# Kernel tuning notes

Measured on AMD Instinct MI355X. Metric: run time of the kernel, lower is better.

The kernel has to match this reference:

```python
import jax, jax.numpy as jnp
import numpy as np

WIN = 16
HEADS = 4


def _window_partition(x, win):
    B, H, W, C = x.shape
    x = x.reshape(B, H // win, win, W // win, win, C)
    x = x.transpose(0, 1, 3, 2, 4, 5)
    return x.reshape(-1, win * win, C)


def _reverse_window_partition(x, win, H, W):
    N, _, C = x.shape
    x = x.reshape(-1, H // win, W // win, win, win, C)
    x = x.transpose(0, 1, 3, 2, 4, 5)
    return x.reshape(-1, H, W, C)


def setup_inputs() -> dict:
    key = jax.random.key(0)
    ks = jax.random.split(key, 7)
    B, H, W, C = 2, 256, 256, 96
    s = 0.02
    return {
        "x": jax.random.normal(ks[0], (B, H, W, C), jnp.float32),
        "qkv_w": jax.random.normal(ks[1], (C, 3 * C), jnp.float32) * s,
        "qkv_b": jax.random.normal(ks[2], (3 * C,), jnp.float32) * s,
        "pe_w": jax.random.normal(ks[3], (3, 3, 1, C), jnp.float32) * s,  # depthwise HWIO
        "pe_b": jax.random.normal(ks[4], (C,), jnp.float32) * s,
        "out_w": jax.random.normal(ks[5], (C, C), jnp.float32) * s,
        "out_b": jax.random.normal(ks[6], (C,), jnp.float32) * s,
    }


def reference(x, qkv_w, qkv_b, pe_w, pe_b, out_w, out_b):
    B, H, W, C = x.shape
    win, heads = WIN, HEADS
    hd = C // heads

    z = _window_partition(x, win)
    N, S, _ = z.shape

    qkv = z @ qkv_w + qkv_b                       # (N, S, 3C)
    # headify then chunk(3): each head's 3*hd channels split into q,k,v
    qkv = qkv.reshape(N, S, heads, 3, hd).transpose(0, 2, 3, 1, 4)  # (N, h, 3, S, hd)
    q, k, v = qkv[:, :, 0], qkv[:, :, 1], qkv[:, :, 2]

    # Locally-enhanced PE: depthwise 3x3 conv on de-headified v
    v_img = v.transpose(0, 2, 1, 3).reshape(N, win, win, C)  # NHWC
    lepe = jax.lax.conv_general_dilated(
        v_img, pe_w, (1, 1), 'SAME',
        dimension_numbers=('NHWC', 'HWIO', 'NHWC'),
        feature_group_count=C) + pe_b
    lepe = lepe.reshape(N, S, heads, hd).transpose(0, 2, 1, 3)  # (N, h, S, hd)

    # per-window SDPA (default scale 1/sqrt(hd))
    scale = 1.0 / jnp.sqrt(jnp.asarray(hd, x.dtype))
    attn = jax.nn.softmax(jnp.einsum('nhsd,nhtd->nhst', q, k) * scale, axis=-1)
    o = jnp.einsum('nhst,nhtd->nhsd', attn, v) + lepe

    o = o.transpose(0, 2, 1, 3).reshape(N, S, C)
    o = _reverse_window_partition(o, win, H, W)   # (B, H, W, C)
    return o @ out_w + out_b
```

## Files before the change

### kernel.cpp

```cpp
#include <hip/hip_runtime.h>


typedef __attribute__((ext_vector_type(8))) short bf16x8;
typedef __attribute__((ext_vector_type(4))) float f32x4;

#define MFMA(a, b, c) __builtin_amdgcn_mfma_f32_16x16x32_bf16(a, b, c, 0, 0, 0)

#if __has_builtin(__builtin_amdgcn_exp2f)
#define EXP2F(x) __builtin_amdgcn_exp2f(x)
#else
#define EXP2F(x) exp2f(x)
#endif

#define SCALE2 (0.20412414523193154f * 1.4426950408889634f)

#define OFF_WT   0u
#define OFF_B2   55296u
#define OFF_WTO  56448u
#define OFF_Q    75904u
#define OFF_K    25241728u
#define OFF_VT   50407552u

__device__ __forceinline__ unsigned short f2bf(float f) {
    union { float f; unsigned int u; } v; v.f = f;
    unsigned int u = v.u;
    return (unsigned short)((u + 0x7FFFu + ((u >> 16) & 1u)) >> 16);
}
__device__ __forceinline__ float bf2f(unsigned short h) {
    union { unsigned int u; float f; } v; v.u = ((unsigned int)h) << 16;
    return v.f;
}
__device__ __forceinline__ unsigned int pk2bf(float a, float b) {
#if __has_builtin(__builtin_amdgcn_cvt_pk_bf16_f32)
    auto p = __builtin_amdgcn_cvt_pk_bf16_f32(a, b);
    union { decltype(p) v; unsigned int u; } cv; cv.v = p;
    return cv.u;
#else
    return (unsigned int)f2bf(a) | ((unsigned int)f2bf(b) << 16);
#endif
}
__device__ __forceinline__ float frcp(float x) {
#if __has_builtin(__builtin_amdgcn_rcpf)
    return __builtin_amdgcn_rcpf(x);
#else
    return 1.0f / x;
#endif
}

__global__ void prep_kernel(const float* __restrict__ qkv_w,
                            const float* __restrict__ qkv_b,
                            const float* __restrict__ out_w,
                            unsigned short* __restrict__ wt,
                            float* __restrict__ b2,
                            unsigned short* __restrict__ wto) {
    const int stride = gridDim.x * 256;
    int i0 = blockIdx.x * 256 + threadIdx.x;
    for (int i = i0; i < 288 * 96; i += stride) {
        const int c = i / 96, k = i % 96;
        float v = qkv_w[k * 288 + c];
        if ((c % 72) < 24) v *= SCALE2;
        wt[i] = f2bf(v);
    }
    for (int i = i0; i < 288; i += stride) {
        float v = qkv_b[i];
        if ((i % 72) < 24) v *= SCALE2;
        b2[i] = v;
    }
    for (int i = i0; i < 96 * 96; i += stride) {
        const int c = i / 96, k = i % 96;
        wto[i] = f2bf(out_w[k * 96 + c]);
    }
}

__launch_bounds__(256, 4)
__global__ void qkv_kernel(const float* __restrict__ x,
                           const unsigned short* __restrict__ wt,
                           const float* __restrict__ b2,
                           unsigned short* __restrict__ Qb,
                           unsigned short* __restrict__ Kb,
                           unsigned short* __restrict__ VTb) {
    __shared__ unsigned short z[128 * 104];
    const int blk = blockIdx.x;
    const int n = blk >> 1, half = blk & 1;
    const int T0 = half << 7;
    const int tid = threadIdx.x;
    const int bW = n >> 8, hy = (n >> 4) & 15, wx = n & 15;

    for (int i = tid; i < 128 * 24; i += 256) {
        const int tl = i / 24, c4 = i % 24;
        const int tok = T0 + tl;
        const int y = tok >> 4, xx = tok & 15;
        const size_t row = (size_t)((bW * 256 + hy * 16 + y) * 256 + wx * 16 + xx);
        const float4 v = *(const float4*)(x + row * 96 + c4 * 4);
        uint2 pk; pk.x = pk2bf(v.x, v.y); pk.y = pk2bf(v.z, v.w);
        *(uint2*)&z[tl * 104 + c4 * 4] = pk;
    }
    __syncthreads();

    const int w = tid >> 6, l = tid & 63;
    const int lm = l & 15, lq = l >> 4;

    bf16x8 af[3][3];
#pragma unroll
    for (int mt = 0; mt < 3; mt++)
#pragma unroll
        for (int ks = 0; ks < 3; ks++)
            af[mt][ks] = *(const bf16x8*)(wt + (w * 72 + mt * 16 + lm) * 96 + ks * 32 + lq * 8);

    for (int nt = 0; nt < 8; nt++) {
        bf16x8 bz[3];
#pragma unroll
        for (int ks = 0; ks < 3; ks++)
            bz[ks] = *(const bf16x8*)&z[(nt * 16 + lm) * 104 + ks * 32 + lq * 8];
#pragma unroll
        for (int mt = 0; mt < 3; mt++) {
            f32x4 acc = {0.f, 0.f, 0.f, 0.f};
#pragma unroll
            for (int ks = 0; ks < 3; ks++) acc = MFMA(af[mt][ks], bz[ks], acc);
            const int r48 = mt * 16 + lq * 4;
            const float4 bias = *(const float4*)(b2 + w * 72 + r48);
            const int kind = r48 / 24, idx = r48 % 24;
            const int tok = T0 + nt * 16 + lm;
            uint2 pk;
            pk.x = pk2bf(acc[0] + bias.x, acc[1] + bias.y);
            pk.y = pk2bf(acc[2] + bias.z, acc[3] + bias.w);
            unsigned short* dst = kind ? Kb : Qb;
            *(uint2*)(dst + ((size_t)(n * 4 + w) * 256 + tok) * 24 + idx) = pk;
        }
    }

#pragma unroll
    for (int tt2 = 0; tt2 < 2; tt2++) {
        const int gtt = w * 2 + tt2;
        bf16x8 az[3];
#pragma unroll
        for (int ks = 0; ks < 3; ks++)
            az[ks] = *(const bf16x8*)&z[(gtt * 16 + lm) * 104 + ks * 32 + lq * 8];
#pragma unroll
        for (int nv = 0; nv < 6; nv++) {
            const int j = nv * 16 + lm;
            const int vrow = (j / 24) * 72 + 48 + (j % 24);
            f32x4 acc = {0.f, 0.f, 0.f, 0.f};
#pragma unroll
            for (int ks = 0; ks < 3; ks++) {
                const bf16x8 bw = *(const bf16x8*)(wt + vrow * 96 + ks * 32 + lq * 8);
                acc = MFMA(az[ks], bw, acc);
            }
            const float bv = b2[vrow];
            const int tokb = T0 + gtt * 16 + lq * 4;
            uint2 pk;
            pk.x = pk2bf(acc[0] + bv, acc[1] + bv);
            pk.y = pk2bf(acc[2] + bv, acc[3] + bv);
            *(uint2*)(VTb + ((size_t)(n * 4 + j / 24) * 24 + (j % 24)) * 256 + tokb) = pk;
        }
    }
}

__launch_bounds__(256, 2)
__global__ void attn_out_kernel(const unsigned short* __restrict__ Qb,
                                const unsigned short* __restrict__ Kb,
                                const unsigned short* __restrict__ VTb,
                                const float* __restrict__ pe_w,
                                const float* __restrict__ pe_b,
                                const unsigned short* __restrict__ wto,
                                const float* __restrict__ out_b,
                                float* __restrict__ out) {
    __shared__ unsigned short sVT[32 * 264];
    __shared__ unsigned short sPO[4 * 64 * 40];
    __shared__ float sPW[216];
    __shared__ float sPB[24];

    const int n = blockIdx.x, tid = threadIdx.x;
    const int w = tid >> 6, l = tid & 63;
    const int lm = l & 15, lq = l >> 4;
    const int qbase = w * 64;
    unsigned short* Pw = &sPO[w * 64 * 40];

    f32x4 oacc[4][6];
#pragma unroll
    for (int b = 0; b < 4; b++)
#pragma unroll
        for (int nt = 0; nt < 6; nt++) oacc[b][nt] = (f32x4){0.f, 0.f, 0.f, 0.f};

    for (int h = 0; h < 4; h++) {
        const size_t nh = (size_t)(n * 4 + h);
        __syncthreads();
        for (int i = tid; i < 24 * 64; i += 256) {
            const int row = i >> 6, c = i & 63;
            *(ushort4*)&sVT[row * 264 + c * 4] =
                *(const ushort4*)(VTb + (nh * 24 + row) * 256 + c * 4);
        }
        if (tid < 64) {
            ushort4 ones; ones.x = ones.y = ones.z = ones.w = (unsigned short)0x3F80;
            *(ushort4*)&sVT[24 * 264 + tid * 4] = ones;
        }
        for (int i = tid; i < 216; i += 256) sPW[i] = pe_w[(i / 24) * 96 + h * 24 + (i % 24)];
        if (tid < 24) sPB[tid] = pe_b[h * 24 + tid];

        bf16x8 qf[4];
#pragma unroll
        for (int b = 0; b < 4; b++) {
            bf16x8 qv = *(const bf16x8*)(Qb + (nh * 256 + qbase + b * 16 + lm) * 24 + lq * 8);
            if (lq == 3) qv = (bf16x8)(short)0;
            qf[b] = qv;
        }
        __syncthreads();

        f32x4 oa[4][2];
#pragma unroll
        for (int b = 0; b < 4; b++)
#pragma unroll
            for (int c = 0; c < 2; c++) oa[b][c] = (f32x4){0.f, 0.f, 0.f, 0.f};

        bf16x8 kfn[2];
#pragma unroll
        for (int a = 0; a < 2; a++)
            kfn[a] = *(const bf16x8*)(Kb + (nh * 256 + a * 16 + lm) * 24 + lq * 8);

        for (int kc = 0; kc < 8; kc++) {
            bf16x8 kfc[2] = {kfn[0], kfn[1]};
            if (kc < 7) {
#pragma unroll
                for (int a = 0; a < 2; a++)
                    kfn[a] = *(const bf16x8*)(Kb + (nh * 256 + (kc + 1) * 32 + a * 16 + lm) * 24 + lq * 8);
            }
#pragma unroll
            for (int a = 0; a < 2; a++) {
                f32x4 s[4];
#pragma unroll
                for (int b = 0; b < 4; b++)
                    s[b] = MFMA(kfc[a], qf[b], ((f32x4){0.f, 0.f, 0.f, 0.f}));
#pragma unroll
                for (int b = 0; b < 4; b++) {
                    uint2 pk;
                    pk.x = pk2bf(EXP2F(s[b][0]), EXP2F(s[b][1]));
                    pk.y = pk2bf(EXP2F(s[b][2]), EXP2F(s[b][3]));
                    *(uint2*)&Pw[(b * 16 + lm) * 40 + a * 16 + lq * 4] = pk;
                }
            }
            bf16x8 vb[2];
#pragma unroll
            for (int c = 0; c < 2; c++)
                vb[c] = *(const bf16x8*)&sVT[(c * 16 + lm) * 264 + kc * 32 + lq * 8];
#pragma unroll
            for (int b = 0; b < 4; b++) {
                const bf16x8 pa = *(const bf16x8*)&Pw[(b * 16 + lm) * 40 + lq * 8];
#pragma unroll
                for (int c = 0; c < 2; c++) oa[b][c] = MFMA(pa, vb[c], oa[b][c]);
            }
        }

        {
            uint4 zz = {0u, 0u, 0u, 0u};
            *(uint4*)&Pw[l * 40 + 24] = zz;
        }
        float w9[2][9], pb2[2];
#pragma unroll
        for (int c = 0; c < 2; c++) {
            const int ch = c * 16 + lm;
            if (ch < 24) {
#pragma unroll
                for (int ta = 0; ta < 9; ta++) w9[c][ta] = sPW[ta * 24 + ch];
                pb2[c] = sPB[ch];
            }
        }
#pragma unroll
        for (int b = 0; b < 4; b++) {
            float rinv[4];
#pragma unroll
            for (int r = 0; r < 4; r++)
                rinv[r] = frcp(__shfl(oa[b][1][r], (l & 48) | 8, 64));
            const int y = w * 4 + b;
            const int x0 = lq * 4;
#pragma unroll
            for (int c = 0; c < 2; c++) {
                const int ch = c * 16 + lm;
                if (ch < 24) {
                    float lep[4] = {pb2[c], pb2[c], pb2[c], pb2[c]};
                    const unsigned short* vbase = &sVT[ch * 264];
#pragma unroll
                    for (int dy = -1; dy <= 1; dy++) {
                        const int ny = y + dy;
                        if ((unsigned)ny > 15u) continue;
                        const unsigned short* vrow = vbase + ny * 16;
                        const float wl = w9[c][(dy + 1) * 3 + 0];
                        const float wm = w9[c][(dy + 1) * 3 + 1];
                        const float wr = w9[c][(dy + 1) * 3 + 2];
#pragma unroll
                        for (int d = -1; d <= 4; d++) {
                            const int xx = x0 + d;
                            if ((unsigned)xx > 15u) continue;
                            const float v = bf2f(vrow[xx]);
                            if (d - 1 >= 0 && d - 1 <= 3) lep[d - 1] = fmaf(v, wr, lep[d - 1]);
                            if (d >= 0 && d <= 3)         lep[d]     = fmaf(v, wm, lep[d]);
                            if (d + 1 <= 3)               lep[d + 1] = fmaf(v, wl, lep[d + 1]);
                        }
                    }
#pragma unroll
                    for (int r = 0; r < 4; r++) {
                        const float val = oa[b][c][r] * rinv[r] + lep[r];
                        Pw[(b * 16 + lq * 4 + r) * 40 + ch] = f2bf(val);
                    }
                }
            }
        }

        bf16x8 aO[4];
#pragma unroll
        for (int b = 0; b < 4; b++)
            aO[b] = *(const bf16x8*)&Pw[(b * 16 + lm) * 40 + lq * 8];
#pragma unroll
        for (int nt = 0; nt < 6; nt++) {
            const bf16x8 bwf = *(const bf16x8*)(wto + (nt * 16 + lm) * 96 + h * 24 + lq * 8);
#pragma unroll
            for (int b = 0; b < 4; b++) oacc[b][nt] = MFMA(aO[b], bwf, oacc[b][nt]);
        }
    }

    const int bW = n >> 8, hy = (n >> 4) & 15, wx = n & 15;
#pragma unroll
    for (int nt = 0; nt < 6; nt++) {
        const float bias = out_b[nt * 16 + lm];
#pragma unroll
        for (int b = 0; b < 4; b++) {
#pragma unroll
            for (int r = 0; r < 4; r++) {
                const int t = qbase + b * 16 + lq * 4 + r;
                const size_t grow =
                    (size_t)((bW * 256 + hy * 16 + (t >> 4)) * 256 + wx * 16 + (t & 15));
                out[grow * 96 + nt * 16 + lm] = oacc[b][nt][r] + bias;
            }
        }
    }
}

extern "C" void kernel_launch(void* const* d_in, const int* in_sizes, int n_in,
                              void* d_out, int out_size, void* d_ws, size_t ws_size,
                              hipStream_t stream) {
    const float* x     = (const float*)d_in[0];
    const float* qkv_w = (const float*)d_in[1];
    const float* qkv_b = (const float*)d_in[2];
    const float* pe_w  = (const float*)d_in[3];
    const float* pe_b  = (const float*)d_in[4];
    const float* out_w = (const float*)d_in[5];
    const float* out_b = (const float*)d_in[6];
    float* out = (float*)d_out;

    char* ws = (char*)d_ws;
    unsigned short* wt  = (unsigned short*)(ws + OFF_WT);
    float*          b2  = (float*)(ws + OFF_B2);
    unsigned short* wto = (unsigned short*)(ws + OFF_WTO);
    unsigned short* Qb  = (unsigned short*)(ws + OFF_Q);
    unsigned short* Kb  = (unsigned short*)(ws + OFF_K);
    unsigned short* VTb = (unsigned short*)(ws + OFF_VT);

    prep_kernel<<<72, 256, 0, stream>>>(qkv_w, qkv_b, out_w, wt, b2, wto);
    qkv_kernel<<<1024, 256, 0, stream>>>(x, wt, b2, Qb, Kb, VTb);
    attn_out_kernel<<<512, 256, 0, stream>>>(Qb, Kb, VTb, pe_w, pe_b, wto, out_b, out);
}
```

Baseline: 201.1 us.

## Fuse QKV projection into attention kernel, keeping Q/K/V in shared memory

Removes the separate qkv_kernel and its global-memory round trip for Q, K and V^T. Each attention block now loads its window of x into registers as bf16 fragments and computes per-head Q, K and V with MFMA. The results go straight into shared-memory buffers used by the attention loop. This avoids writing and re-reading roughly 75 MB of intermediates and one kernel launch. In exchange it adds shared-memory and register pressure, plus redundant weight loads per head inside the block, which may lower occupancy.

```diff
diff --git a/kernel.cpp b/kernel.cpp
--- a/kernel.cpp
+++ b/kernel.cpp
@@ -17,9 +17,6 @@
 #define OFF_WT   0u
 #define OFF_B2   55296u
 #define OFF_WTO  56448u
-#define OFF_Q    75904u
-#define OFF_K    25241728u
-#define OFF_VT   50407552u
 
 __device__ __forceinline__ unsigned short f2bf(float f) {
     union { float f; unsigned int u; } v; v.f = f;
@@ -72,99 +69,17 @@
     }
 }
 
-__launch_bounds__(256, 4)
-__global__ void qkv_kernel(const float* __restrict__ x,
-                           const unsigned short* __restrict__ wt,
-                           const float* __restrict__ b2,
-                           unsigned short* __restrict__ Qb,
-                           unsigned short* __restrict__ Kb,
-                           unsigned short* __restrict__ VTb) {
-    __shared__ unsigned short z[128 * 104];
-    const int blk = blockIdx.x;
-    const int n = blk >> 1, half = blk & 1;
-    const int T0 = half << 7;
-    const int tid = threadIdx.x;
-    const int bW = n >> 8, hy = (n >> 4) & 15, wx = n & 15;
-
-    for (int i = tid; i < 128 * 24; i += 256) {
-        const int tl = i / 24, c4 = i % 24;
-        const int tok = T0 + tl;
-        const int y = tok >> 4, xx = tok & 15;
-        const size_t row = (size_t)((bW * 256 + hy * 16 + y) * 256 + wx * 16 + xx);
-        const float4 v = *(const float4*)(x + row * 96 + c4 * 4);
-        uint2 pk; pk.x = pk2bf(v.x, v.y); pk.y = pk2bf(v.z, v.w);
-        *(uint2*)&z[tl * 104 + c4 * 4] = pk;
-    }
-    __syncthreads();
-
-    const int w = tid >> 6, l = tid & 63;
-    const int lm = l & 15, lq = l >> 4;
-
-    bf16x8 af[3][3];
-#pragma unroll
-    for (int mt = 0; mt < 3; mt++)
-#pragma unroll
-        for (int ks = 0; ks < 3; ks++)
-            af[mt][ks] = *(const bf16x8*)(wt + (w * 72 + mt * 16 + lm) * 96 + ks * 32 + lq * 8);
-
-    for (int nt = 0; nt < 8; nt++) {
-        bf16x8 bz[3];
-#pragma unroll
-        for (int ks = 0; ks < 3; ks++)
-            bz[ks] = *(const bf16x8*)&z[(nt * 16 + lm) * 104 + ks * 32 + lq * 8];
-#pragma unroll
-        for (int mt = 0; mt < 3; mt++) {
-            f32x4 acc = {0.f, 0.f, 0.f, 0.f};
-#pragma unroll
-            for (int ks = 0; ks < 3; ks++) acc = MFMA(af[mt][ks], bz[ks], acc);
-            const int r48 = mt * 16 + lq * 4;
-            const float4 bias = *(const float4*)(b2 + w * 72 + r48);
-            const int kind = r48 / 24, idx = r48 % 24;
-            const int tok = T0 + nt * 16 + lm;
-            uint2 pk;
-            pk.x = pk2bf(acc[0] + bias.x, acc[1] + bias.y);
-            pk.y = pk2bf(acc[2] + bias.z, acc[3] + bias.w);
-            unsigned short* dst = kind ? Kb : Qb;
-            *(uint2*)(dst + ((size_t)(n * 4 + w) * 256 + tok) * 24 + idx) = pk;
-        }
-    }
-
-#pragma unroll
-    for (int tt2 = 0; tt2 < 2; tt2++) {
-        const int gtt = w * 2 + tt2;
-        bf16x8 az[3];
-#pragma unroll
-        for (int ks = 0; ks < 3; ks++)
-            az[ks] = *(const bf16x8*)&z[(gtt * 16 + lm) * 104 + ks * 32 + lq * 8];
-#pragma unroll
-        for (int nv = 0; nv < 6; nv++) {
-            const int j = nv * 16 + lm;
-            const int vrow = (j / 24) * 72 + 48 + (j % 24);
-            f32x4 acc = {0.f, 0.f, 0.f, 0.f};
-#pragma unroll
-            for (int ks = 0; ks < 3; ks++) {
-                const bf16x8 bw = *(const bf16x8*)(wt + vrow * 96 + ks * 32 + lq * 8);
-                acc = MFMA(az[ks], bw, acc);
-            }
-            const float bv = b2[vrow];
-            const int tokb = T0 + gtt * 16 + lq * 4;
-            uint2 pk;
-            pk.x = pk2bf(acc[0] + bv, acc[1] + bv);
-            pk.y = pk2bf(acc[2] + bv, acc[3] + bv);
-            *(uint2*)(VTb + ((size_t)(n * 4 + j / 24) * 24 + (j % 24)) * 256 + tokb) = pk;
-        }
-    }
-}
-
 __launch_bounds__(256, 2)
-__global__ void attn_out_kernel(const unsigned short* __restrict__ Qb,
-                                const unsigned short* __restrict__ Kb,
-                                const unsigned short* __restrict__ VTb,
-                                const float* __restrict__ pe_w,
-                                const float* __restrict__ pe_b,
-                                const unsigned short* __restrict__ wto,
-                                const float* __restrict__ out_b,
-                                float* __restrict__ out) {
+__global__ void fused_kernel(const float* __restrict__ x,
+                             const unsigned short* __restrict__ wt,
+                             const float* __restrict__ b2,
+                             const float* __restrict__ pe_w,
+                             const float* __restrict__ pe_b,
+                             const unsigned short* __restrict__ wto,
+                             const float* __restrict__ out_b,
+                             float* __restrict__ out) {
+    __shared__ unsigned short sQp[4][64 * 24 + 16];
+    __shared__ unsigned short sK[256 * 24 + 8];
     __shared__ unsigned short sVT[32 * 264];
     __shared__ unsigned short sPO[4 * 64 * 40];
     __shared__ float sPW[216];
@@ -173,9 +88,31 @@
     const int n = blockIdx.x, tid = threadIdx.x;
     const int w = tid >> 6, l = tid & 63;
     const int lm = l & 15, lq = l >> 4;
-    const int qbase = w * 64;
+    const int bW = n >> 8, hy = (n >> 4) & 15, wx = n & 15;
     unsigned short* Pw = &sPO[w * 64 * 40];
 
+    if (tid < 64) {
+        ushort4 ones; ones.x = ones.y = ones.z = ones.w = (unsigned short)0x3F80;
+        *(ushort4*)&sVT[24 * 264 + tid * 4] = ones;
+    }
+
+    bf16x8 zf[4][3];
+#pragma unroll
+    for (int t4 = 0; t4 < 4; t4++) {
+        const int y = w * 4 + t4;
+        const size_t grow = (size_t)((bW * 256 + hy * 16 + y) * 256 + wx * 16 + lm);
+        const float* xr = x + grow * 96 + lq * 8;
+#pragma unroll
+        for (int ks = 0; ks < 3; ks++) {
+            const float4 p0 = *(const float4*)(xr + ks * 32);
+            const float4 p1 = *(const float4*)(xr + ks * 32 + 4);
+            union { unsigned int u[4]; bf16x8 v; } cv;
+            cv.u[0] = pk2bf(p0.x, p0.y); cv.u[1] = pk2bf(p0.z, p0.w);
+            cv.u[2] = pk2bf(p1.x, p1.y); cv.u[3] = pk2bf(p1.z, p1.w);
+            zf[t4][ks] = cv.v;
+        }
+    }
+
     f32x4 oacc[4][6];
 #pragma unroll
     for (int b = 0; b < 4; b++)
@@ -183,28 +120,65 @@
         for (int nt = 0; nt < 6; nt++) oacc[b][nt] = (f32x4){0.f, 0.f, 0.f, 0.f};
 
     for (int h = 0; h < 4; h++) {
-        const size_t nh = (size_t)(n * 4 + h);
         __syncthreads();
-        for (int i = tid; i < 24 * 64; i += 256) {
-            const int row = i >> 6, c = i & 63;
-            *(ushort4*)&sVT[row * 264 + c * 4] =
-                *(const ushort4*)(VTb + (nh * 24 + row) * 256 + c * 4);
-        }
-        if (tid < 64) {
-            ushort4 ones; ones.x = ones.y = ones.z = ones.w = (unsigned short)0x3F80;
-            *(ushort4*)&sVT[24 * 264 + tid * 4] = ones;
-        }
+
+#pragma unroll
+        for (int mt = 0; mt < 3; mt++) {
+            bf16x8 af[3];
+#pragma unroll
+            for (int ks = 0; ks < 3; ks++)
+                af[ks] = *(const bf16x8*)(wt + (h * 72 + mt * 16 + lm) * 96 + ks * 32 + lq * 8);
+            const int r48 = mt * 16 + lq * 4;
+            const float4 bias = *(const float4*)(b2 + h * 72 + r48);
+#pragma unroll
+            for (int t4 = 0; t4 < 4; t4++) {
+                f32x4 acc = {0.f, 0.f, 0.f, 0.f};
+#pragma unroll
+                for (int ks = 0; ks < 3; ks++) acc = MFMA(af[ks], zf[t4][ks], acc);
+                uint2 pk;
+                pk.x = pk2bf(acc[0] + bias.x, acc[1] + bias.y);
+                pk.y = pk2bf(acc[2] + bias.z, acc[3] + bias.w);
+                const int tl = t4 * 16 + lm;
+                if (r48 < 24) *(uint2*)&sQp[w][tl * 24 + r48] = pk;
+                else          *(uint2*)&sK[(w * 64 + tl) * 24 + (r48 - 24)] = pk;
+            }
+        }
+
+#pragma unroll
+        for (int nv = 0; nv < 2; nv++) {
+            const int ch = nv * 16 + lm;
+            const int vrow = h * 72 + 48 + (ch < 24 ? ch : 23);
+            bf16x8 bw[3];
+#pragma unroll
+            for (int ks = 0; ks < 3; ks++)
+                bw[ks] = *(const bf16x8*)(wt + vrow * 96 + ks * 32 + lq * 8);
+            const float bv = b2[vrow];
+#pragma unroll
+            for (int t4 = 0; t4 < 4; t4++) {
+                f32x4 acc = {0.f, 0.f, 0.f, 0.f};
+#pragma unroll
+                for (int ks = 0; ks < 3; ks++) acc = MFMA(zf[t4][ks], bw[ks], acc);
+                if (ch < 24) {
+                    uint2 pk;
+                    pk.x = pk2bf(acc[0] + bv, acc[1] + bv);
+                    pk.y = pk2bf(acc[2] + bv, acc[3] + bv);
+                    *(uint2*)&sVT[ch * 264 + w * 64 + t4 * 16 + lq * 4] = pk;
+                }
+            }
+        }
+
         for (int i = tid; i < 216; i += 256) sPW[i] = pe_w[(i / 24) * 96 + h * 24 + (i % 24)];
         if (tid < 24) sPB[tid] = pe_b[h * 24 + tid];
 
+        __syncthreads();
+
         bf16x8 qf[4];
 #pragma unroll
         for (int b = 0; b < 4; b++) {
-            bf16x8 qv = *(const bf16x8*)(Qb + (nh * 256 + qbase + b * 16 + lm) * 24 + lq * 8);
+            bf16x8 qv = *(const bf16x8*)&sQp[w][(b * 16 + lm) * 24 + lq * 8];
             if (lq == 3) qv = (bf16x8)(short)0;
             qf[b] = qv;
         }
-        __syncthreads();
 
         f32x4 oa[4][2];
 #pragma unroll
@@ -212,18 +186,11 @@
 #pragma unroll
             for (int c = 0; c < 2; c++) oa[b][c] = (f32x4){0.f, 0.f, 0.f, 0.f};
 
-        bf16x8 kfn[2];
-#pragma unroll
-        for (int a = 0; a < 2; a++)
-            kfn[a] = *(const bf16x8*)(Kb + (nh * 256 + a * 16 + lm) * 24 + lq * 8);
-
         for (int kc = 0; kc < 8; kc++) {
-            bf16x8 kfc[2] = {kfn[0], kfn[1]};
-            if (kc < 7) {
-#pragma unroll
-                for (int a = 0; a < 2; a++)
-                    kfn[a] = *(const bf16x8*)(Kb + (nh * 256 + (kc + 1) * 32 + a * 16 + lm) * 24 + lq * 8);
-            }
+            bf16x8 kfc[2];
+#pragma unroll
+            for (int a = 0; a < 2; a++)
+                kfc[a] = *(const bf16x8*)&sK[(kc * 32 + a * 16 + lm) * 24 + lq * 8];
 #pragma unroll
             for (int a = 0; a < 2; a++) {
                 f32x4 s[4];
@@ -317,7 +284,6 @@
         }
     }
 
-    const int bW = n >> 8, hy = (n >> 4) & 15, wx = n & 15;
 #pragma unroll
     for (int nt = 0; nt < 6; nt++) {
         const float bias = out_b[nt * 16 + lm];
@@ -325,7 +291,7 @@
         for (int b = 0; b < 4; b++) {
 #pragma unroll
             for (int r = 0; r < 4; r++) {
-                const int t = qbase + b * 16 + lq * 4 + r;
+                const int t = w * 64 + b * 16 + lq * 4 + r;
                 const size_t grow =
                     (size_t)((bW * 256 + hy * 16 + (t >> 4)) * 256 + wx * 16 + (t & 15));
                 out[grow * 96 + nt * 16 + lm] = oacc[b][nt][r] + bias;
@@ -350,11 +316,7 @@
     unsigned short* wt  = (unsigned short*)(ws + OFF_WT);
     float*          b2  = (float*)(ws + OFF_B2);
     unsigned short* wto = (unsigned short*)(ws + OFF_WTO);
-    unsigned short* Qb  = (unsigned short*)(ws + OFF_Q);
-    unsigned short* Kb  = (unsigned short*)(ws + OFF_K);
-    unsigned short* VTb = (unsigned short*)(ws + OFF_VT);
 
     prep_kernel<<<72, 256, 0, stream>>>(qkv_w, qkv_b, out_w, wt, b2, wto);
-    qkv_kernel<<<1024, 256, 0, stream>>>(x, wt, b2, Qb, Kb, VTb);
-    attn_out_kernel<<<512, 256, 0, stream>>>(Qb, Kb, VTb, pe_w, pe_b, wto, out_b, out);
-}
+    fused_kernel<<<512, 256, 0, stream>>>(x, wt, b2, pe_w, pe_b, wto, out_b, out);
+}
```

Result: slower. 207.9 us (+3.4%).
